# Performance work log

Hardware: AMD Instinct MI355X
Metric: run time of the kernel (lower is better)

The kernel has to match this reference:

```python
import jax, jax.numpy as jnp
import numpy as np
import math

B, S, D, H = 4, 1024, 1024, 16
HD = D // H          # 64
ROT = 32             # min(head_dim, 32)


def _rope(q, k, freqs):
    # q, k: [B,H,S,HD]; freqs: [ROT//2]
    rd = 2 * freqs.shape[0]
    s = q.shape[2]
    pos = jnp.arange(s, dtype=jnp.float32)
    emb = pos[:, None] * freqs[None, :]            # [S, rd/2]
    cos = jnp.cos(emb)[None, None, :, :]           # [1,1,S,rd/2]
    sin = jnp.sin(emb)[None, None, :, :]

    def rot(x):
        xr, xp = x[..., :rd], x[..., rd:]
        xr = xr.reshape(*xr.shape[:-1], rd // 2, 2)
        x0 = xr[..., 0] * cos - xr[..., 1] * sin
        x1 = xr[..., 1] * cos + xr[..., 0] * sin
        xr = jnp.stack([x0, x1], axis=-1).reshape(*x.shape[:-1], rd)
        return jnp.concatenate([xr, xp], axis=-1)

    return rot(q), rot(k)


def setup_inputs() -> dict:
    key = jax.random.key(0)
    ks = jax.random.split(key, 16)
    lin = lambda k: jax.random.normal(k, (D, D), jnp.float32) * 0.02
    inp = {
        'real': jax.random.normal(ks[0], (B, S, D), jnp.float32),
        'imag': jax.random.normal(ks[1], (B, S, D), jnp.float32),
        'attention_mask': jnp.zeros((B, S), dtype=bool),
        'wq_r': lin(ks[2]), 'bq_r': jnp.zeros((D,), jnp.float32),
        'wk_r': lin(ks[3]), 'bk_r': jnp.zeros((D,), jnp.float32),
        'wv_r': lin(ks[4]), 'bv_r': jnp.zeros((D,), jnp.float32),
        'wq_i': lin(ks[5]), 'bq_i': jnp.zeros((D,), jnp.float32),
        'wk_i': lin(ks[6]), 'bk_i': jnp.zeros((D,), jnp.float32),
        'wv_i': lin(ks[7]), 'bv_i': jnp.zeros((D,), jnp.float32),
        'wo_r': lin(ks[8]), 'bo_r': jnp.zeros((D,), jnp.float32),
        'wo_i': lin(ks[9]), 'bo_i': jnp.zeros((D,), jnp.float32),
        'phase_shifts': jax.random.normal(ks[10], (H, HD), jnp.float32) * 0.02,
        'entanglement': jnp.eye(H, dtype=jnp.float32)
                        + jax.random.normal(ks[11], (H, H), jnp.float32) * 0.01,
        'rotary_freqs': (10000.0 ** (-jnp.arange(0, ROT, 2, dtype=jnp.float32) / ROT)),
        'interference_strength': jnp.ones((1,), jnp.float32),
        'attention_temperature': jnp.ones((1,), jnp.float32),
    }
    return inp


def reference(real, imag, attention_mask,
              wq_r, bq_r, wk_r, bk_r, wv_r, bv_r,
              wq_i, bq_i, wk_i, bk_i, wv_i, bv_i,
              wo_r, bo_r, wo_i, bo_i,
              phase_shifts, entanglement, rotary_freqs,
              interference_strength, attention_temperature):
    b, s, d = real.shape
    h, hd = phase_shifts.shape

    def proj(x, w, bias):  # [B,S,D] -> [B,H,S,HD]
        return (x @ w + bias).reshape(b, s, h, hd).transpose(0, 2, 1, 3)

    q_r = proj(real, wq_r, bq_r); k_r = proj(real, wk_r, bk_r); v_r = proj(real, wv_r, bv_r)
    q_i = proj(imag, wq_i, bq_i); k_i = proj(imag, wk_i, bk_i); v_i = proj(imag, wv_i, bv_i)

    q_r, k_r = _rope(q_r, k_r, rotary_freqs)
    q_i, k_i = _rope(q_i, k_i, rotary_freqs)

    # entanglement mixing across heads
    q_r = jnp.einsum('bhsd,hx->bxsd', q_r, entanglement)
    q_i = jnp.einsum('bhsd,hx->bxsd', q_i, entanglement)
    k_r = jnp.einsum('bhsd,hx->bxsd', k_r, entanglement)
    k_i = jnp.einsum('bhsd,hx->bxsd', k_i, entanglement)

    pc = jnp.cos(phase_shifts)[None, :, None, :]   # [1,H,1,HD]
    ps = jnp.sin(phase_shifts)[None, :, None, :]
    qr, qi = q_r * pc - q_i * ps, q_r * ps + q_i * pc
    kr, ki = k_r * pc - k_i * ps, k_r * ps + k_i * pc

    scale = 1.0 / math.sqrt(hd)
    attn_r = (jnp.einsum('bhqd,bhkd->bhqk', qr, kr)
              + jnp.einsum('bhqd,bhkd->bhqk', qi, ki)) * scale
    attn_i = (jnp.einsum('bhqd,bhkd->bhqk', qi, kr)
              - jnp.einsum('bhqd,bhkd->bhqk', qr, ki)) * scale
    attn_mag = jnp.sqrt(attn_r ** 2 + attn_i ** 2 + 1e-6)

    causal = jnp.triu(jnp.ones((s, s), dtype=bool), 1)[None, None]       # [1,1,S,S]
    final_mask = causal | attention_mask[:, None, None, :]               # [B,1,S,S]

    temp = jnp.maximum(attention_temperature, 0.01)
    strength = jax.nn.sigmoid(interference_strength)
    logits = jnp.where(final_mask, -jnp.inf, attn_mag * strength / temp)
    attn_w = jax.nn.softmax(logits, axis=-1)

    out_r = jnp.einsum('bhqk,bhkd->bhqd', attn_w, v_r).transpose(0, 2, 1, 3).reshape(b, s, d)
    out_i = jnp.einsum('bhqk,bhkd->bhqd', attn_w, v_i).transpose(0, 2, 1, 3).reshape(b, s, d)
    out_r = out_r @ wo_r + bo_r
    out_i = out_i @ wo_i + bo_i
    return out_r, out_i
```

## Files before the change

### kernel.cpp

```cpp
#include <hip/hip_runtime.h>
#include <hip/hip_bf16.h>


typedef __attribute__((ext_vector_type(8))) short bf16x8;
typedef __attribute__((ext_vector_type(4))) short bf16x4;
typedef __attribute__((ext_vector_type(4))) float f32x4;

#define DEV static __device__ __forceinline__

DEV short f2b(float f) {
    __hip_bfloat16 h = __float2bfloat16(f);
    short s; __builtin_memcpy(&s, &h, 2); return s;
}
DEV float b2f(short s) {
    unsigned u = ((unsigned)(unsigned short)s) << 16;
    float f; __builtin_memcpy(&f, &u, 4); return f;
}

DEV f32x4 mfma(bf16x8 a, bf16x8 b, f32x4 c) {
    return __builtin_amdgcn_mfma_f32_16x16x32_bf16(a, b, c, 0, 0, 0);
}

DEV void gload16(const void* g, void* l) {
    __builtin_amdgcn_global_load_lds(
        (const __attribute__((address_space(1))) void*)g,
        (__attribute__((address_space(3))) void*)l, 16, 0, 0);
}

DEV void storeC(float* C, size_t idx, float v) { C[idx] = v; }
DEV void storeC(short* C, size_t idx, float v) { C[idx] = f2b(v); }

__global__ __launch_bounds__(256) void k_f2b(const float* __restrict__ in0,
                                             const float* __restrict__ in1,
                                             short* __restrict__ out0,
                                             short* __restrict__ out1) {
    const float* in = blockIdx.y ? in1 : in0;
    short* out = blockIdx.y ? out1 : out0;
    int i = (blockIdx.x * 256 + threadIdx.x) * 4;
    float4 v = *reinterpret_cast<const float4*>(&in[i]);
    bf16x4 o;
    o[0] = f2b(v.x); o[1] = f2b(v.y); o[2] = f2b(v.z); o[3] = f2b(v.w);
    *reinterpret_cast<bf16x4*>(&out[i]) = o;
}

__global__ __launch_bounds__(256) void k_tables(const float* __restrict__ freqs,
                                                const float* __restrict__ phase,
                                                float* __restrict__ ropeC,
                                                float* __restrict__ ropeS,
                                                float* __restrict__ phC,
                                                float* __restrict__ phS) {
    int i = blockIdx.x * 256 + threadIdx.x;
    int s = i >> 4, pp = i & 15;
    float a = (float)s * freqs[pp];
    ropeC[i] = cosf(a); ropeS[i] = sinf(a);
    if (i < 1024) { phC[i] = cosf(phase[i]); phS[i] = sinf(phase[i]); }
}

__global__ __launch_bounds__(256) void k_wtrans(
    const float* W0, const float* W1, const float* W2, const float* W3,
    const float* W4, const float* W5, const float* W6, const float* W7,
    short* __restrict__ WtBase) {
    __shared__ short T[64][72];
    int z = blockIdx.z;
    const float* W = z == 0 ? W0 : z == 1 ? W1 : z == 2 ? W2 : z == 3 ? W3
                   : z == 4 ? W4 : z == 5 ? W5 : z == 6 ? W6 : W7;
    short* Wt = WtBase + (size_t)z * 1024 * 1024;
    int n0 = blockIdx.x * 64, k0 = blockIdx.y * 64;
    int t = threadIdx.x;
    for (int i = 0; i < 4; ++i) {
        int idx = t + i * 256; int r = idx >> 4; int c4 = idx & 15;
        float4 v = *reinterpret_cast<const float4*>(&W[(size_t)(k0 + r) * 1024 + n0 + c4 * 4]);
        T[c4 * 4 + 0][r] = f2b(v.x); T[c4 * 4 + 1][r] = f2b(v.y);
        T[c4 * 4 + 2][r] = f2b(v.z); T[c4 * 4 + 3][r] = f2b(v.w);
    }
    __syncthreads();
    for (int i = 0; i < 2; ++i) {
        int idx = t + i * 256; int r = idx >> 3; int c8 = idx & 7;
        bf16x8 v;
        for (int j = 0; j < 8; ++j) v[j] = T[r][c8 * 8 + j];
        *reinterpret_cast<bf16x8*>(&Wt[(size_t)(n0 + r) * 1024 + k0 + c8 * 8]) = v;
    }
}

struct GemmPtrs {
    const short* A[6];
    const short* B[6];
    const float* bias[6];
    void* C[6];
};

template <typename OutT>
__global__ __launch_bounds__(256) void k_gemm(GemmPtrs gp) {
    __shared__ short As[2][128][64];
    __shared__ short Bs[2][128][64];
    int z = blockIdx.z;
    const short* A  = gp.A[z];
    const short* BT = gp.B[z];
    const float* bias = gp.bias[z];
    OutT* C = (OutT*)gp.C[z];

    int t = threadIdx.x;
    int w = t >> 6, l = t & 63;
    int lr = l & 15, lg = l >> 4;
    int wr = w >> 1, wc = w & 1;
    int row0 = blockIdx.y * 128, col0 = blockIdx.x * 128;

    auto stage = [&](int buf, int kt) {
        for (int i = 0; i < 4; ++i) {
            int chunk = i * 256 + t;
            int r = chunk >> 3, j = chunk & 7;
            char* la = (char*)&As[buf][0][0] + (size_t)(i * 256 + w * 64) * 16;
            char* lb = (char*)&Bs[buf][0][0] + (size_t)(i * 256 + w * 64) * 16;
            gload16(&A[(size_t)(row0 + r) * 1024 + kt * 64 + j * 8], la);
            gload16(&BT[(size_t)(col0 + r) * 1024 + kt * 64 + j * 8], lb);
        }
    };

    f32x4 acc[4][4] = {};
    stage(0, 0);
    __syncthreads();
    int cur = 0;
    for (int kt = 0; kt < 16; ++kt) {
        if (kt < 15) stage(cur ^ 1, kt + 1);
        for (int kk = 0; kk < 2; ++kk) {
            bf16x8 af[4], bfr[4];
            for (int m = 0; m < 4; ++m)
                af[m] = *reinterpret_cast<bf16x8*>(&As[cur][wr * 64 + m * 16 + lr][kk * 32 + lg * 8]);
            for (int n = 0; n < 4; ++n)
                bfr[n] = *reinterpret_cast<bf16x8*>(&Bs[cur][wc * 64 + n * 16 + lr][kk * 32 + lg * 8]);
            for (int m = 0; m < 4; ++m)
                for (int n = 0; n < 4; ++n)
                    acc[m][n] = mfma(af[m], bfr[n], acc[m][n]);
        }
        __syncthreads();
        cur ^= 1;
    }
    for (int n = 0; n < 4; ++n) {
        int col = col0 + wc * 64 + n * 16 + lr;
        float bv = bias[col];
        for (int m = 0; m < 4; ++m)
            for (int r = 0; r < 4; ++r) {
                int row = row0 + wr * 64 + m * 16 + lg * 4 + r;
                storeC(C, (size_t)row * 1024 + col, acc[m][n][r] + bv);
            }
    }
}

__global__ __launch_bounds__(256) void k_transform(
    const short* __restrict__ Qr, const short* __restrict__ Qi,
    const short* __restrict__ Kr, const short* __restrict__ Ki,
    const float* __restrict__ ropeC, const float* __restrict__ ropeS,
    const float* __restrict__ phC, const float* __restrict__ phS,
    const float* __restrict__ ent,
    short* __restrict__ oQr, short* __restrict__ oQi,
    short* __restrict__ oKr, short* __restrict__ oKi) {
    __shared__ float xr[1024], xi[1024], E[256];
    int bs = blockIdx.x; int b = bs >> 10; int s = bs & 1023;
    int t = threadIdx.x;
    const short* inR = blockIdx.y ? Kr : Qr;
    const short* inI = blockIdx.y ? Ki : Qi;
    short* outR = blockIdx.y ? oKr : oQr;
    short* outI = blockIdx.y ? oKi : oQi;
    E[t] = ent[t];
    int d0 = t * 4;
    bf16x4 r4 = *reinterpret_cast<const bf16x4*>(&inR[(size_t)bs * 1024 + d0]);
    bf16x4 i4 = *reinterpret_cast<const bf16x4*>(&inI[(size_t)bs * 1024 + d0]);
    float vr[4] = { b2f(r4[0]), b2f(r4[1]), b2f(r4[2]), b2f(r4[3]) };
    float vi[4] = { b2f(i4[0]), b2f(i4[1]), b2f(i4[2]), b2f(i4[3]) };
    if ((d0 & 63) < 32) {
        int p0 = (d0 & 63) >> 1;
        float c0 = ropeC[s * 16 + p0], s0 = ropeS[s * 16 + p0];
        float c1 = ropeC[s * 16 + p0 + 1], s1 = ropeS[s * 16 + p0 + 1];
        float r0, r1;
        r0 = vr[0] * c0 - vr[1] * s0; r1 = vr[1] * c0 + vr[0] * s0; vr[0] = r0; vr[1] = r1;
        r0 = vr[2] * c1 - vr[3] * s1; r1 = vr[3] * c1 + vr[2] * s1; vr[2] = r0; vr[3] = r1;
        r0 = vi[0] * c0 - vi[1] * s0; r1 = vi[1] * c0 + vi[0] * s0; vi[0] = r0; vi[1] = r1;
        r0 = vi[2] * c1 - vi[3] * s1; r1 = vi[3] * c1 + vi[2] * s1; vi[2] = r0; vi[3] = r1;
    }
    for (int j = 0; j < 4; ++j) { xr[d0 + j] = vr[j]; xi[d0 + j] = vi[j]; }
    __syncthreads();
    for (int j = 0; j < 4; ++j) {
        int d = d0 + j; int x = d >> 6; int hd = d & 63;
        float ar = 0.f, ai = 0.f;
        for (int h = 0; h < 16; ++h) {
            float e = E[h * 16 + x];
            ar += xr[h * 64 + hd] * e;
            ai += xi[h * 64 + hd] * e;
        }
        float pc = phC[d], ps = phS[d];
        float outr = ar * pc - ai * ps;
        float outi = ar * ps + ai * pc;
        size_t oidx = ((size_t)(b * 16 + x) * 1024 + s) * 64 + hd;
        outR[oidx] = f2b(outr);
        outI[oidx] = f2b(outi);
    }
}

__global__ __launch_bounds__(256) void k_vtrans(const short* __restrict__ Vr,
                                                const short* __restrict__ Vi,
                                                short* __restrict__ Vtr,
                                                short* __restrict__ Vti) {
    __shared__ short T[64][72];
    int st = blockIdx.x, h = blockIdx.y, b = blockIdx.z;
    int t = threadIdx.x;
    int s0 = st * 64;
    for (int comp = 0; comp < 2; ++comp) {
        const short* V = comp ? Vi : Vr;
        short* Vt = comp ? Vti : Vtr;
        if (comp) __syncthreads();
        for (int i = 0; i < 2; ++i) {
            int idx = t + i * 256; int r = idx >> 3; int c8 = idx & 7;
            bf16x8 v = *reinterpret_cast<const bf16x8*>(
                &V[(size_t)(b * 1024 + s0 + r) * 1024 + h * 64 + c8 * 8]);
            for (int j = 0; j < 8; ++j) T[c8 * 8 + j][r] = v[j];
        }
        __syncthreads();
        for (int i = 0; i < 2; ++i) {
            int idx = t + i * 256; int r = idx >> 3; int c8 = idx & 7;
            bf16x8 v;
            for (int j = 0; j < 8; ++j) v[j] = T[r][c8 * 8 + j];
            *reinterpret_cast<bf16x8*>(
                &Vt[((size_t)(b * 16 + h) * 64 + r) * 1024 + s0 + c8 * 8]) = v;
        }
    }
}

__global__ __launch_bounds__(256) void k_attn(
    const short* __restrict__ Qr, const short* __restrict__ Qi,
    const short* __restrict__ Kr, const short* __restrict__ Ki,
    const short* __restrict__ Vtr, const short* __restrict__ Vti,
    const float* __restrict__ istr, const float* __restrict__ itemp,
    short* __restrict__ Or, short* __restrict__ Oi) {
    __shared__ short Ks_r[64][72], Ks_i[64][72], Vs_r[64][72], Vs_i[64][72];
    __shared__ short Pl[4][16][72];
    int qt = (int)gridDim.x - 1 - blockIdx.x;
    int h = blockIdx.y, b = blockIdx.z;
    int t = threadIdx.x, w = t >> 6, l = t & 63;
    int lr = l & 15, lg = l >> 4;
    float cs = (1.f / (1.f + __expf(-istr[0]))) / fmaxf(itemp[0], 0.01f) * 0.125f;
    const float eps2 = 1e-6f * 64.f;
    int qrow_a = qt * 64 + w * 16 + lr;
    size_t qbase = ((size_t)(b * 16 + h) * 1024 + qrow_a) * 64;
    bf16x8 fqr[2], fqi[2], fnqr[2];
    for (int kk = 0; kk < 2; ++kk) {
        fqr[kk] = *reinterpret_cast<const bf16x8*>(&Qr[qbase + kk * 32 + lg * 8]);
        fqi[kk] = *reinterpret_cast<const bf16x8*>(&Qi[qbase + kk * 32 + lg * 8]);
        for (int j = 0; j < 8; ++j)
            fnqr[kk][j] = (short)(fqr[kk][j] ^ (short)0x8000);
    }
    f32x4 Oacc_r[4] = {}, Oacc_i[4] = {};
    float m[4] = {0.f, 0.f, 0.f, 0.f}, lsum[4] = {0.f, 0.f, 0.f, 0.f};
    size_t kvbase = (size_t)(b * 16 + h) * 1024 * 64;
    int qrow_d = qt * 64 + w * 16 + lg * 4;

    int r0 = t >> 3, c0 = (t & 7) * 8;
    int r1 = r0 + 32;
    bf16x8 gKr0, gKr1, gKi0, gKi1, gVr0, gVr1, gVi0, gVi1;
    auto stage_load = [&](int kt_) {
        const short* Kr_t = Kr + kvbase + (size_t)kt_ * 64 * 64;
        const short* Ki_t = Ki + kvbase + (size_t)kt_ * 64 * 64;
        const short* Vr_t = Vtr + kvbase + kt_ * 64;
        const short* Vi_t = Vti + kvbase + kt_ * 64;
        gKr0 = *reinterpret_cast<const bf16x8*>(&Kr_t[r0 * 64 + c0]);
        gKr1 = *reinterpret_cast<const bf16x8*>(&Kr_t[r1 * 64 + c0]);
        gKi0 = *reinterpret_cast<const bf16x8*>(&Ki_t[r0 * 64 + c0]);
        gKi1 = *reinterpret_cast<const bf16x8*>(&Ki_t[r1 * 64 + c0]);
        gVr0 = *reinterpret_cast<const bf16x8*>(&Vr_t[(size_t)r0 * 1024 + c0]);
        gVr1 = *reinterpret_cast<const bf16x8*>(&Vr_t[(size_t)r1 * 1024 + c0]);
        gVi0 = *reinterpret_cast<const bf16x8*>(&Vi_t[(size_t)r0 * 1024 + c0]);
        gVi1 = *reinterpret_cast<const bf16x8*>(&Vi_t[(size_t)r1 * 1024 + c0]);
    };
    auto stage_write = [&]() {
        *reinterpret_cast<bf16x8*>(&Ks_r[r0][c0]) = gKr0;
        *reinterpret_cast<bf16x8*>(&Ks_r[r1][c0]) = gKr1;
        *reinterpret_cast<bf16x8*>(&Ks_i[r0][c0]) = gKi0;
        *reinterpret_cast<bf16x8*>(&Ks_i[r1][c0]) = gKi1;
        *reinterpret_cast<bf16x8*>(&Vs_r[r0][c0]) = gVr0;
        *reinterpret_cast<bf16x8*>(&Vs_r[r1][c0]) = gVr1;
        *reinterpret_cast<bf16x8*>(&Vs_i[r0][c0]) = gVi0;
        *reinterpret_cast<bf16x8*>(&Vs_i[r1][c0]) = gVi1;
    };

    stage_load(0); stage_write();
    __syncthreads();
    for (int kt = 0; kt <= qt; ++kt) {
        if (kt < qt) stage_load(kt + 1);
        f32x4 sr[4] = {}, si[4] = {};
        for (int cg = 0; cg < 4; ++cg) {
            for (int kk = 0; kk < 2; ++kk) {
                bf16x8 fkr = *reinterpret_cast<bf16x8*>(&Ks_r[cg * 16 + lr][kk * 32 + lg * 8]);
                bf16x8 fki = *reinterpret_cast<bf16x8*>(&Ks_i[cg * 16 + lr][kk * 32 + lg * 8]);
                sr[cg] = mfma(fqr[kk], fkr, sr[cg]);
                sr[cg] = mfma(fqi[kk], fki, sr[cg]);
                si[cg] = mfma(fqi[kk], fkr, si[cg]);
                si[cg] = mfma(fnqr[kk], fki, si[cg]);
            }
        }
        float lgt[4][4];
        for (int cg = 0; cg < 4; ++cg)
            for (int r = 0; r < 4; ++r)
                lgt[cg][r] = cs * sqrtf(sr[cg][r] * sr[cg][r] + si[cg][r] * si[cg][r] + eps2);
        if (kt == qt) {
            for (int cg = 0; cg < 4; ++cg) {
                int kcol = kt * 64 + cg * 16 + lr;
                for (int r = 0; r < 4; ++r)
                    if (kcol > qrow_d + r) lgt[cg][r] = -__builtin_inff();
            }
        }
        float alpha[4];
        for (int r = 0; r < 4; ++r) {
            float v = fmaxf(fmaxf(lgt[0][r], lgt[1][r]), fmaxf(lgt[2][r], lgt[3][r]));
            v = fmaxf(v, __shfl_xor(v, 1)); v = fmaxf(v, __shfl_xor(v, 2));
            v = fmaxf(v, __shfl_xor(v, 4)); v = fmaxf(v, __shfl_xor(v, 8));
            float mn = fmaxf(m[r], v);
            alpha[r] = __expf(m[r] - mn);
            m[r] = mn;
        }
        float psum[4] = {0.f, 0.f, 0.f, 0.f};
        for (int cg = 0; cg < 4; ++cg)
            for (int r = 0; r < 4; ++r) {
                float p = __expf(lgt[cg][r] - m[r]);
                psum[r] += p;
                Pl[w][lg * 4 + r][cg * 16 + lr] = f2b(p);
            }
        for (int r = 0; r < 4; ++r) {
            float v = psum[r];
            v += __shfl_xor(v, 1); v += __shfl_xor(v, 2);
            v += __shfl_xor(v, 4); v += __shfl_xor(v, 8);
            lsum[r] = lsum[r] * alpha[r] + v;
        }
        for (int cg = 0; cg < 4; ++cg)
            for (int r = 0; r < 4; ++r) { Oacc_r[cg][r] *= alpha[r]; Oacc_i[cg][r] *= alpha[r]; }
        for (int kk = 0; kk < 2; ++kk) {
            bf16x8 fp = *reinterpret_cast<bf16x8*>(&Pl[w][lr][kk * 32 + lg * 8]);
            for (int cg = 0; cg < 4; ++cg) {
                bf16x8 fvr = *reinterpret_cast<bf16x8*>(&Vs_r[cg * 16 + lr][kk * 32 + lg * 8]);
                bf16x8 fvi = *reinterpret_cast<bf16x8*>(&Vs_i[cg * 16 + lr][kk * 32 + lg * 8]);
                Oacc_r[cg] = mfma(fp, fvr, Oacc_r[cg]);
                Oacc_i[cg] = mfma(fp, fvi, Oacc_i[cg]);
            }
        }
        if (kt < qt) {
            __syncthreads();
            stage_write();
            __syncthreads();
        }
    }
    for (int cg = 0; cg < 4; ++cg)
        for (int r = 0; r < 4; ++r) {
            int q = qrow_d + r;
            float inv = 1.f / lsum[r];
            size_t oidx = ((size_t)(b * 1024 + q)) * 1024 + h * 64 + cg * 16 + lr;
            Or[oidx] = f2b(Oacc_r[cg][r] * inv);
            Oi[oidx] = f2b(Oacc_i[cg][r] * inv);
        }
}

extern "C" void kernel_launch(void* const* d_in, const int* in_sizes, int n_in,
                              void* d_out, int out_size, void* d_ws, size_t ws_size,
                              hipStream_t stream) {
    (void)in_sizes; (void)n_in; (void)out_size; (void)ws_size;
    const float* real = (const float*)d_in[0];
    const float* imag = (const float*)d_in[1];
    const float* W[8]    = { (const float*)d_in[3],  (const float*)d_in[5],  (const float*)d_in[7],
                             (const float*)d_in[9],  (const float*)d_in[11], (const float*)d_in[13],
                             (const float*)d_in[15], (const float*)d_in[17] };
    const float* bias[8] = { (const float*)d_in[4],  (const float*)d_in[6],  (const float*)d_in[8],
                             (const float*)d_in[10], (const float*)d_in[12], (const float*)d_in[14],
                             (const float*)d_in[16], (const float*)d_in[18] };
    const float* phase = (const float*)d_in[19];
    const float* ent   = (const float*)d_in[20];
    const float* freqs = (const float*)d_in[21];
    const float* istr  = (const float*)d_in[22];
    const float* itemp = (const float*)d_in[23];
    float* out = (float*)d_out;

    char* p = (char*)d_ws;
    const size_t MB = 1024 * 1024;
    short* Wt  = (short*)(p + 0);
    short* Xr  = (short*)(p + 16 * MB);
    short* Xi  = (short*)(p + 24 * MB);
    short* Qr  = (short*)(p + 32 * MB);
    short* Kr  = (short*)(p + 40 * MB);
    short* Qi  = (short*)(p + 48 * MB);
    short* Ki  = (short*)(p + 56 * MB);
    short* Vr  = (short*)(p + 64 * MB);
    short* Vi  = (short*)(p + 72 * MB);
    short* tQr = (short*)(p + 80 * MB);
    short* tQi = (short*)(p + 88 * MB);
    short* tKr = (short*)(p + 96 * MB);
    short* tKi = (short*)(p + 104 * MB);
    short* Vtr = (short*)(p + 112 * MB);
    short* Vti = (short*)(p + 120 * MB);
    short* Obr = (short*)(p + 128 * MB);
    short* Obi = (short*)(p + 136 * MB);
    float* ropeC = (float*)(p + 144 * MB);
    float* ropeS = (float*)(p + 144 * MB + 65536);
    float* phC   = (float*)(p + 144 * MB + 131072);
    float* phS   = (float*)(p + 144 * MB + 135168);

    dim3 blk(256);
    k_f2b<<<dim3(4096, 2), blk, 0, stream>>>(real, imag, Xr, Xi);
    k_tables<<<dim3(64), blk, 0, stream>>>(freqs, phase, ropeC, ropeS, phC, phS);
    k_wtrans<<<dim3(16, 16, 8), blk, 0, stream>>>(W[0], W[1], W[2], W[3],
                                                  W[4], W[5], W[6], W[7], Wt);
    GemmPtrs gpP;
    gpP.A[0] = Xr; gpP.A[1] = Xr; gpP.A[2] = Xr;
    gpP.A[3] = Xi; gpP.A[4] = Xi; gpP.A[5] = Xi;
    for (int i = 0; i < 6; ++i) { gpP.B[i] = Wt + (size_t)i * MB; gpP.bias[i] = bias[i]; }
    gpP.C[0] = Qr; gpP.C[1] = Kr; gpP.C[2] = Vr;
    gpP.C[3] = Qi; gpP.C[4] = Ki; gpP.C[5] = Vi;
    k_gemm<short><<<dim3(8, 32, 6), blk, 0, stream>>>(gpP);
    k_transform<<<dim3(4096, 2), blk, 0, stream>>>(Qr, Qi, Kr, Ki,
                                                   ropeC, ropeS, phC, phS, ent,
                                                   tQr, tQi, tKr, tKi);
    k_vtrans<<<dim3(16, 16, 4), blk, 0, stream>>>(Vr, Vi, Vtr, Vti);
    k_attn<<<dim3(16, 16, 4), blk, 0, stream>>>(tQr, tQi, tKr, tKi, Vtr, Vti,
                                                istr, itemp, Obr, Obi);
    GemmPtrs gpO;
    gpO.A[0] = Obr; gpO.A[1] = Obi;
    gpO.B[0] = Wt + 6 * MB; gpO.B[1] = Wt + 7 * MB;
    gpO.bias[0] = bias[6]; gpO.bias[1] = bias[7];
    gpO.C[0] = out; gpO.C[1] = out + 4 * MB;
    for (int i = 2; i < 6; ++i) { gpO.A[i] = Obi; gpO.B[i] = Wt + 7 * MB; gpO.bias[i] = bias[7]; gpO.C[i] = out + 4 * MB; }
    k_gemm<float><<<dim3(8, 32, 2), blk, 0, stream>>>(gpO);
}
```

Baseline: 445.2 us.

## Fold head entanglement into Q/K weights, widen attention tiles, simplify GEMM staging

Head entanglement mixing is folded into the Q and K projection weights and biases by new precompute kernels, so the per-token transform kernel only applies RoPE and the phase rotation and writes vectorized outputs without shared memory. This relies on RoPE commuting with the cross-head linear mix. The attention kernel now uses 512 threads and 128 query rows per block, so each K/V tile is shared by twice as many queries. A per-wave diagonal check skips fully masked tiles. The GEMM drops its double-buffered 64-wide K tiles for single-buffered 32-wide tiles with two barriers per step, which lowers LDS use but removes the load/compute overlap.

```diff
diff --git a/kernel.cpp b/kernel.cpp
--- a/kernel.cpp
+++ b/kernel.cpp
@@ -43,17 +43,52 @@
     *reinterpret_cast<bf16x4*>(&out[i]) = o;
 }
 
-__global__ __launch_bounds__(256) void k_tables(const float* __restrict__ freqs,
-                                                const float* __restrict__ phase,
-                                                float* __restrict__ ropeC,
-                                                float* __restrict__ ropeS,
-                                                float* __restrict__ phC,
-                                                float* __restrict__ phS) {
+__global__ __launch_bounds__(256) void k_tables(
+    const float* __restrict__ freqs, const float* __restrict__ phase,
+    const float* __restrict__ ent,
+    const float* bq_r, const float* bk_r, const float* bq_i, const float* bk_i,
+    float* __restrict__ ropeC, float* __restrict__ ropeS,
+    float* __restrict__ phC, float* __restrict__ phS,
+    float* __restrict__ biasF) {
     int i = blockIdx.x * 256 + threadIdx.x;
     int s = i >> 4, pp = i & 15;
     float a = (float)s * freqs[pp];
     ropeC[i] = cosf(a); ropeS[i] = sinf(a);
     if (i < 1024) { phC[i] = cosf(phase[i]); phS[i] = sinf(phase[i]); }
+    if (i < 4096) {
+        int z = i >> 10, d = i & 1023;
+        const float* bz = z == 0 ? bq_r : z == 1 ? bk_r : z == 2 ? bq_i : bk_i;
+        int x = d >> 6, hd = d & 63;
+        float acc = 0.f;
+        for (int h = 0; h < 16; ++h) acc += bz[h * 64 + hd] * ent[h * 16 + x];
+        biasF[i] = acc;
+    }
+}
+
+__global__ __launch_bounds__(256) void k_efold(
+    const float* W0, const float* W1, const float* W2, const float* W3,
+    const float* __restrict__ ent, float* __restrict__ outBase) {
+    __shared__ float row[1024];
+    __shared__ float E[256];
+    int z = blockIdx.y;
+    const float* W = z == 0 ? W0 : z == 1 ? W1 : z == 2 ? W2 : W3;
+    float* out = outBase + (size_t)z * 1024 * 1024;
+    int k = blockIdx.x;
+    int t = threadIdx.x;
+    E[t] = ent[t];
+    *reinterpret_cast<float4*>(&row[t * 4]) =
+        *reinterpret_cast<const float4*>(&W[(size_t)k * 1024 + t * 4]);
+    __syncthreads();
+    float4 o;
+    float res[4];
+    for (int j = 0; j < 4; ++j) {
+        int d = t * 4 + j; int x = d >> 6; int hd = d & 63;
+        float acc = 0.f;
+        for (int h = 0; h < 16; ++h) acc += row[h * 64 + hd] * E[h * 16 + x];
+        res[j] = acc;
+    }
+    o.x = res[0]; o.y = res[1]; o.z = res[2]; o.w = res[3];
+    *reinterpret_cast<float4*>(&out[(size_t)k * 1024 + t * 4]) = o;
 }
 
 __global__ __launch_bounds__(256) void k_wtrans(
@@ -91,8 +126,8 @@
 
 template <typename OutT>
 __global__ __launch_bounds__(256) void k_gemm(GemmPtrs gp) {
-    __shared__ short As[2][128][64];
-    __shared__ short Bs[2][128][64];
+    __shared__ short As[128][32];
+    __shared__ short Bs[128][32];
     int z = blockIdx.z;
     const short* A  = gp.A[z];
     const short* BT = gp.B[z];
@@ -105,35 +140,26 @@
     int wr = w >> 1, wc = w & 1;
     int row0 = blockIdx.y * 128, col0 = blockIdx.x * 128;
 
-    auto stage = [&](int buf, int kt) {
-        for (int i = 0; i < 4; ++i) {
+    f32x4 acc[4][4] = {};
+    for (int k0 = 0; k0 < 1024; k0 += 32) {
+        __syncthreads();
+        for (int i = 0; i < 2; ++i) {
             int chunk = i * 256 + t;
-            int r = chunk >> 3, j = chunk & 7;
-            char* la = (char*)&As[buf][0][0] + (size_t)(i * 256 + w * 64) * 16;
-            char* lb = (char*)&Bs[buf][0][0] + (size_t)(i * 256 + w * 64) * 16;
-            gload16(&A[(size_t)(row0 + r) * 1024 + kt * 64 + j * 8], la);
-            gload16(&BT[(size_t)(col0 + r) * 1024 + kt * 64 + j * 8], lb);
-        }
-    };
-
-    f32x4 acc[4][4] = {};
-    stage(0, 0);
-    __syncthreads();
-    int cur = 0;
-    for (int kt = 0; kt < 16; ++kt) {
-        if (kt < 15) stage(cur ^ 1, kt + 1);
-        for (int kk = 0; kk < 2; ++kk) {
-            bf16x8 af[4], bfr[4];
-            for (int m = 0; m < 4; ++m)
-                af[m] = *reinterpret_cast<bf16x8*>(&As[cur][wr * 64 + m * 16 + lr][kk * 32 + lg * 8]);
+            int r = chunk >> 2, c4 = chunk & 3;
+            char* la = (char*)&As[0][0] + (size_t)(i * 256 + w * 64) * 16;
+            char* lb = (char*)&Bs[0][0] + (size_t)(i * 256 + w * 64) * 16;
+            gload16(&A[(size_t)(row0 + r) * 1024 + k0 + c4 * 8], la);
+            gload16(&BT[(size_t)(col0 + r) * 1024 + k0 + c4 * 8], lb);
+        }
+        __syncthreads();
+        bf16x8 af[4], bfr[4];
+        for (int m = 0; m < 4; ++m)
+            af[m] = *reinterpret_cast<bf16x8*>(&As[wr * 64 + m * 16 + lr][lg * 8]);
+        for (int n = 0; n < 4; ++n)
+            bfr[n] = *reinterpret_cast<bf16x8*>(&Bs[wc * 64 + n * 16 + lr][lg * 8]);
+        for (int m = 0; m < 4; ++m)
             for (int n = 0; n < 4; ++n)
-                bfr[n] = *reinterpret_cast<bf16x8*>(&Bs[cur][wc * 64 + n * 16 + lr][kk * 32 + lg * 8]);
-            for (int m = 0; m < 4; ++m)
-                for (int n = 0; n < 4; ++n)
-                    acc[m][n] = mfma(af[m], bfr[n], acc[m][n]);
-        }
-        __syncthreads();
-        cur ^= 1;
+                acc[m][n] = mfma(af[m], bfr[n], acc[m][n]);
     }
     for (int n = 0; n < 4; ++n) {
         int col = col0 + wc * 64 + n * 16 + lr;
@@ -151,17 +177,14 @@
     const short* __restrict__ Kr, const short* __restrict__ Ki,
     const float* __restrict__ ropeC, const float* __restrict__ ropeS,
     const float* __restrict__ phC, const float* __restrict__ phS,
-    const float* __restrict__ ent,
     short* __restrict__ oQr, short* __restrict__ oQi,
     short* __restrict__ oKr, short* __restrict__ oKi) {
-    __shared__ float xr[1024], xi[1024], E[256];
     int bs = blockIdx.x; int b = bs >> 10; int s = bs & 1023;
     int t = threadIdx.x;
     const short* inR = blockIdx.y ? Kr : Qr;
     const short* inI = blockIdx.y ? Ki : Qi;
     short* outR = blockIdx.y ? oKr : oQr;
     short* outI = blockIdx.y ? oKi : oQi;
-    E[t] = ent[t];
     int d0 = t * 4;
     bf16x4 r4 = *reinterpret_cast<const bf16x4*>(&inR[(size_t)bs * 1024 + d0]);
     bf16x4 i4 = *reinterpret_cast<const bf16x4*>(&inI[(size_t)bs * 1024 + d0]);
@@ -177,23 +200,17 @@
         r0 = vi[0] * c0 - vi[1] * s0; r1 = vi[1] * c0 + vi[0] * s0; vi[0] = r0; vi[1] = r1;
         r0 = vi[2] * c1 - vi[3] * s1; r1 = vi[3] * c1 + vi[2] * s1; vi[2] = r0; vi[3] = r1;
     }
-    for (int j = 0; j < 4; ++j) { xr[d0 + j] = vr[j]; xi[d0 + j] = vi[j]; }
-    __syncthreads();
+    bf16x4 oR, oI;
     for (int j = 0; j < 4; ++j) {
-        int d = d0 + j; int x = d >> 6; int hd = d & 63;
-        float ar = 0.f, ai = 0.f;
-        for (int h = 0; h < 16; ++h) {
-            float e = E[h * 16 + x];
-            ar += xr[h * 64 + hd] * e;
-            ai += xi[h * 64 + hd] * e;
-        }
+        int d = d0 + j;
         float pc = phC[d], ps = phS[d];
-        float outr = ar * pc - ai * ps;
-        float outi = ar * ps + ai * pc;
-        size_t oidx = ((size_t)(b * 16 + x) * 1024 + s) * 64 + hd;
-        outR[oidx] = f2b(outr);
-        outI[oidx] = f2b(outi);
-    }
+        oR[j] = f2b(vr[j] * pc - vi[j] * ps);
+        oI[j] = f2b(vr[j] * ps + vi[j] * pc);
+    }
+    int x = d0 >> 6, hd0 = d0 & 63;
+    size_t oidx = ((size_t)(b * 16 + x) * 1024 + s) * 64 + hd0;
+    *reinterpret_cast<bf16x4*>(&outR[oidx]) = oR;
+    *reinterpret_cast<bf16x4*>(&outI[oidx]) = oI;
 }
 
 __global__ __launch_bounds__(256) void k_vtrans(const short* __restrict__ Vr,
@@ -225,21 +242,21 @@
     }
 }
 
-__global__ __launch_bounds__(256) void k_attn(
+__global__ __launch_bounds__(512) void k_attn(
     const short* __restrict__ Qr, const short* __restrict__ Qi,
     const short* __restrict__ Kr, const short* __restrict__ Ki,
     const short* __restrict__ Vtr, const short* __restrict__ Vti,
     const float* __restrict__ istr, const float* __restrict__ itemp,
     short* __restrict__ Or, short* __restrict__ Oi) {
     __shared__ short Ks_r[64][72], Ks_i[64][72], Vs_r[64][72], Vs_i[64][72];
-    __shared__ short Pl[4][16][72];
+    __shared__ short Pl[8][16][72];
     int qt = (int)gridDim.x - 1 - blockIdx.x;
     int h = blockIdx.y, b = blockIdx.z;
     int t = threadIdx.x, w = t >> 6, l = t & 63;
     int lr = l & 15, lg = l >> 4;
     float cs = (1.f / (1.f + __expf(-istr[0]))) / fmaxf(itemp[0], 0.01f) * 0.125f;
     const float eps2 = 1e-6f * 64.f;
-    int qrow_a = qt * 64 + w * 16 + lr;
+    int qrow_a = qt * 128 + w * 16 + lr;
     size_t qbase = ((size_t)(b * 16 + h) * 1024 + qrow_a) * 64;
     bf16x8 fqr[2], fqi[2], fnqr[2];
     for (int kk = 0; kk < 2; ++kk) {
@@ -251,96 +268,91 @@
     f32x4 Oacc_r[4] = {}, Oacc_i[4] = {};
     float m[4] = {0.f, 0.f, 0.f, 0.f}, lsum[4] = {0.f, 0.f, 0.f, 0.f};
     size_t kvbase = (size_t)(b * 16 + h) * 1024 * 64;
-    int qrow_d = qt * 64 + w * 16 + lg * 4;
+    int qrow_d = qt * 128 + w * 16 + lg * 4;
+    int kt_diag = (qt * 128 + w * 16) >> 6;
+    int ktmax = 2 * qt + 1;
 
     int r0 = t >> 3, c0 = (t & 7) * 8;
-    int r1 = r0 + 32;
-    bf16x8 gKr0, gKr1, gKi0, gKi1, gVr0, gVr1, gVi0, gVi1;
+    bf16x8 gKr, gKi, gVr, gVi;
     auto stage_load = [&](int kt_) {
         const short* Kr_t = Kr + kvbase + (size_t)kt_ * 64 * 64;
         const short* Ki_t = Ki + kvbase + (size_t)kt_ * 64 * 64;
         const short* Vr_t = Vtr + kvbase + kt_ * 64;
         const short* Vi_t = Vti + kvbase + kt_ * 64;
-        gKr0 = *reinterpret_cast<const bf16x8*>(&Kr_t[r0 * 64 + c0]);
-        gKr1 = *reinterpret_cast<const bf16x8*>(&Kr_t[r1 * 64 + c0]);
-        gKi0 = *reinterpret_cast<const bf16x8*>(&Ki_t[r0 * 64 + c0]);
-        gKi1 = *reinterpret_cast<const bf16x8*>(&Ki_t[r1 * 64 + c0]);
-        gVr0 = *reinterpret_cast<const bf16x8*>(&Vr_t[(size_t)r0 * 1024 + c0]);
-        gVr1 = *reinterpret_cast<const bf16x8*>(&Vr_t[(size_t)r1 * 1024 + c0]);
-        gVi0 = *reinterpret_cast<const bf16x8*>(&Vi_t[(size_t)r0 * 1024 + c0]);
-        gVi1 = *reinterpret_cast<const bf16x8*>(&Vi_t[(size_t)r1 * 1024 + c0]);
+        gKr = *reinterpret_cast<const bf16x8*>(&Kr_t[r0 * 64 + c0]);
+        gKi = *reinterpret_cast<const bf16x8*>(&Ki_t[r0 * 64 + c0]);
+        gVr = *reinterpret_cast<const bf16x8*>(&Vr_t[(size_t)r0 * 1024 + c0]);
+        gVi = *reinterpret_cast<const bf16x8*>(&Vi_t[(size_t)r0 * 1024 + c0]);
     };
     auto stage_write = [&]() {
-        *reinterpret_cast<bf16x8*>(&Ks_r[r0][c0]) = gKr0;
-        *reinterpret_cast<bf16x8*>(&Ks_r[r1][c0]) = gKr1;
-        *reinterpret_cast<bf16x8*>(&Ks_i[r0][c0]) = gKi0;
-        *reinterpret_cast<bf16x8*>(&Ks_i[r1][c0]) = gKi1;
-        *reinterpret_cast<bf16x8*>(&Vs_r[r0][c0]) = gVr0;
-        *reinterpret_cast<bf16x8*>(&Vs_r[r1][c0]) = gVr1;
-        *reinterpret_cast<bf16x8*>(&Vs_i[r0][c0]) = gVi0;
-        *reinterpret_cast<bf16x8*>(&Vs_i[r1][c0]) = gVi1;
+        *reinterpret_cast<bf16x8*>(&Ks_r[r0][c0]) = gKr;
+        *reinterpret_cast<bf16x8*>(&Ks_i[r0][c0]) = gKi;
+        *reinterpret_cast<bf16x8*>(&Vs_r[r0][c0]) = gVr;
+        *reinterpret_cast<bf16x8*>(&Vs_i[r0][c0]) = gVi;
     };
 
     stage_load(0); stage_write();
     __syncthreads();
-    for (int kt = 0; kt <= qt; ++kt) {
-        if (kt < qt) stage_load(kt + 1);
-        f32x4 sr[4] = {}, si[4] = {};
-        for (int cg = 0; cg < 4; ++cg) {
+    for (int kt = 0; kt <= ktmax; ++kt) {
+        if (kt < ktmax) stage_load(kt + 1);
+        if (kt <= kt_diag) {
+            f32x4 sr[4] = {}, si[4] = {};
+            for (int cg = 0; cg < 4; ++cg) {
+                for (int kk = 0; kk < 2; ++kk) {
+                    bf16x8 fkr = *reinterpret_cast<bf16x8*>(&Ks_r[cg * 16 + lr][kk * 32 + lg * 8]);
+                    bf16x8 fki = *reinterpret_cast<bf16x8*>(&Ks_i[cg * 16 + lr][kk * 32 + lg * 8]);
+                    sr[cg] = mfma(fqr[kk], fkr, sr[cg]);
+                    sr[cg] = mfma(fqi[kk], fki, sr[cg]);
+                    si[cg] = mfma(fqi[kk], fkr, si[cg]);
+                    si[cg] = mfma(fnqr[kk], fki, si[cg]);
+                }
+            }
+            float lgt[4][4];
+            for (int cg = 0; cg < 4; ++cg)
+                for (int r = 0; r < 4; ++r)
+                    lgt[cg][r] = cs * sqrtf(sr[cg][r] * sr[cg][r] + si[cg][r] * si[cg][r] + eps2);
+            if (kt == kt_diag) {
+                for (int cg = 0; cg < 4; ++cg) {
+                    int kcol = kt * 64 + cg * 16 + lr;
+                    for (int r = 0; r < 4; ++r)
+                        if (kcol > qrow_d + r) lgt[cg][r] = -__builtin_inff();
+                }
+            }
+            float alpha[4];
+            for (int r = 0; r < 4; ++r) {
+                float v = fmaxf(fmaxf(lgt[0][r], lgt[1][r]), fmaxf(lgt[2][r], lgt[3][r]));
+                v = fmaxf(v, __shfl_xor(v, 1)); v = fmaxf(v, __shfl_xor(v, 2));
+                v = fmaxf(v, __shfl_xor(v, 4)); v = fmaxf(v, __shfl_xor(v, 8));
+                float mn = fmaxf(m[r], v);
+                alpha[r] = __expf(m[r] - mn);
+                m[r] = mn;
+            }
+            float psum[4] = {0.f, 0.f, 0.f, 0.f};
+            for (int cg = 0; cg < 4; ++cg)
+                for (int r = 0; r < 4; ++r) {
+                    float p = __expf(lgt[cg][r] - m[r]);
+                    psum[r] += p;
+                    Pl[w][lg * 4 + r][cg * 16 + lr] = f2b(p);
+                }
+            for (int r = 0; r < 4; ++r) {
+                float v = psum[r];
+                v += __shfl_xor(v, 1); v += __shfl_xor(v, 2);
+                v += __shfl_xor(v, 4); v += __shfl_xor(v, 8);
+                lsum[r] = lsum[r] * alpha[r] + v;
+            }
+            for (int cg = 0; cg < 4; ++cg)
+                for (int r = 0; r < 4; ++r) { Oacc_r[cg][r] *= alpha[r]; Oacc_i[cg][r] *= alpha[r]; }
             for (int kk = 0; kk < 2; ++kk) {
-                bf16x8 fkr = *reinterpret_cast<bf16x8*>(&Ks_r[cg * 16 + lr][kk * 32 + lg * 8]);
-                bf16x8 fki = *reinterpret_cast<bf16x8*>(&Ks_i[cg * 16 + lr][kk * 32 + lg * 8]);
-                sr[cg] = mfma(fqr[kk], fkr, sr[cg]);
-                sr[cg] = mfma(fqi[kk], fki, sr[cg]);
-                si[cg] = mfma(fqi[kk], fkr, si[cg]);
-                si[cg] = mfma(fnqr[kk], fki, si[cg]);
-            }
-        }
-        float lgt[4][4];
-        for (int cg = 0; cg < 4; ++cg)
-            for (int r = 0; r < 4; ++r)
-                lgt[cg][r] = cs * sqrtf(sr[cg][r] * sr[cg][r] + si[cg][r] * si[cg][r] + eps2);
-        if (kt == qt) {
-            for (int cg = 0; cg < 4; ++cg) {
-                int kcol = kt * 64 + cg * 16 + lr;
-                for (int r = 0; r < 4; ++r)
-                    if (kcol > qrow_d + r) lgt[cg][r] = -__builtin_inff();
-            }
-        }
-        float alpha[4];
-        for (int r = 0; r < 4; ++r) {
-            float v = fmaxf(fmaxf(lgt[0][r], lgt[1][r]), fmaxf(lgt[2][r], lgt[3][r]));
-            v = fmaxf(v, __shfl_xor(v, 1)); v = fmaxf(v, __shfl_xor(v, 2));
-            v = fmaxf(v, __shfl_xor(v, 4)); v = fmaxf(v, __shfl_xor(v, 8));
-            float mn = fmaxf(m[r], v);
-            alpha[r] = __expf(m[r] - mn);
-            m[r] = mn;
-        }
-        float psum[4] = {0.f, 0.f, 0.f, 0.f};
-        for (int cg = 0; cg < 4; ++cg)
-            for (int r = 0; r < 4; ++r) {
-                float p = __expf(lgt[cg][r] - m[r]);
-                psum[r] += p;
-                Pl[w][lg * 4 + r][cg * 16 + lr] = f2b(p);
-            }
-        for (int r = 0; r < 4; ++r) {
-            float v = psum[r];
-            v += __shfl_xor(v, 1); v += __shfl_xor(v, 2);
-            v += __shfl_xor(v, 4); v += __shfl_xor(v, 8);
-            lsum[r] = lsum[r] * alpha[r] + v;
-        }
-        for (int cg = 0; cg < 4; ++cg)
-            for (int r = 0; r < 4; ++r) { Oacc_r[cg][r] *= alpha[r]; Oacc_i[cg][r] *= alpha[r]; }
-        for (int kk = 0; kk < 2; ++kk) {
-            bf16x8 fp = *reinterpret_cast<bf16x8*>(&Pl[w][lr][kk * 32 + lg * 8]);
-            for (int cg = 0; cg < 4; ++cg) {
-                bf16x8 fvr = *reinterpret_cast<bf16x8*>(&Vs_r[cg * 16 + lr][kk * 32 + lg * 8]);
-                bf16x8 fvi = *reinterpret_cast<bf16x8*>(&Vs_i[cg * 16 + lr][kk * 32 + lg * 8]);
-                Oacc_r[cg] = mfma(fp, fvr, Oacc_r[cg]);
-                Oacc_i[cg] = mfma(fp, fvi, Oacc_i[cg]);
-            }
-        }
-        if (kt < qt) {
+                bf16x8 fp = *reinterpret_cast<bf16x8*>(&Pl[w][lr][kk * 32 + lg * 8]);
+                for (int cg = 0; cg < 4; ++cg) {
+                    bf16x8 fvr = *reinterpret_cast<bf16x8*>(&Vs_r[cg * 16 + lr][kk * 32 + lg * 8]);
+                    bf16x8 fvi = *reinterpret_cast<bf16x8*>(&Vs_i[cg * 16 + lr][kk * 32 + lg * 8]);
+                    Oacc_r[cg] = mfma(fp, fvr, Oacc_r[cg]);
+                    Oacc_i[cg] = mfma(fp, fvi, Oacc_i[cg]);
+                }
+            }
+        }
+        if (kt < ktmax) {
             __syncthreads();
             stage_write();
             __syncthreads();
@@ -398,25 +410,34 @@
     float* ropeS = (float*)(p + 144 * MB + 65536);
     float* phC   = (float*)(p + 144 * MB + 131072);
     float* phS   = (float*)(p + 144 * MB + 135168);
+    float* biasF = (float*)(p + 144 * MB + 139264);
+    float* Wf    = (float*)(p + 146 * MB);
 
     dim3 blk(256);
     k_f2b<<<dim3(4096, 2), blk, 0, stream>>>(real, imag, Xr, Xi);
-    k_tables<<<dim3(64), blk, 0, stream>>>(freqs, phase, ropeC, ropeS, phC, phS);
-    k_wtrans<<<dim3(16, 16, 8), blk, 0, stream>>>(W[0], W[1], W[2], W[3],
-                                                  W[4], W[5], W[6], W[7], Wt);
+    k_tables<<<dim3(64), blk, 0, stream>>>(freqs, phase, ent,
+                                           bias[0], bias[1], bias[3], bias[4],
+                                           ropeC, ropeS, phC, phS, biasF);
+    k_efold<<<dim3(1024, 4), blk, 0, stream>>>(W[0], W[1], W[3], W[4], ent, Wf);
+    k_wtrans<<<dim3(16, 16, 8), blk, 0, stream>>>(
+        Wf + 0 * MB, Wf + 1 * MB, W[2],
+        Wf + 2 * MB, Wf + 3 * MB, W[5],
+        W[6], W[7], Wt);
     GemmPtrs gpP;
     gpP.A[0] = Xr; gpP.A[1] = Xr; gpP.A[2] = Xr;
     gpP.A[3] = Xi; gpP.A[4] = Xi; gpP.A[5] = Xi;
-    for (int i = 0; i < 6; ++i) { gpP.B[i] = Wt + (size_t)i * MB; gpP.bias[i] = bias[i]; }
+    for (int i = 0; i < 6; ++i) gpP.B[i] = Wt + (size_t)i * MB;
+    gpP.bias[0] = biasF + 0; gpP.bias[1] = biasF + 1024; gpP.bias[2] = bias[2];
+    gpP.bias[3] = biasF + 2048; gpP.bias[4] = biasF + 3072; gpP.bias[5] = bias[5];
     gpP.C[0] = Qr; gpP.C[1] = Kr; gpP.C[2] = Vr;
     gpP.C[3] = Qi; gpP.C[4] = Ki; gpP.C[5] = Vi;
     k_gemm<short><<<dim3(8, 32, 6), blk, 0, stream>>>(gpP);
     k_transform<<<dim3(4096, 2), blk, 0, stream>>>(Qr, Qi, Kr, Ki,
-                                                   ropeC, ropeS, phC, phS, ent,
+                                                   ropeC, ropeS, phC, phS,
                                                    tQr, tQi, tKr, tKi);
     k_vtrans<<<dim3(16, 16, 4), blk, 0, stream>>>(Vr, Vi, Vtr, Vti);
-    k_attn<<<dim3(16, 16, 4), blk, 0, stream>>>(tQr, tQi, tKr, tKi, Vtr, Vti,
-                                                istr, itemp, Obr, Obi);
+    k_attn<<<dim3(8, 16, 4), dim3(512), 0, stream>>>(tQr, tQi, tKr, tKi, Vtr, Vti,
+                                                     istr, itemp, Obr, Obi);
     GemmPtrs gpO;
     gpO.A[0] = Obr; gpO.A[1] = Obi;
     gpO.B[0] = Wt + 6 * MB; gpO.B[1] = Wt + 7 * MB;
```

Result: faster. 410.2 us (-7.9%).
